# Optimization experiments

Hardware: AMD Instinct MI355X
Metric: run time of the kernel (lower is better)

Reference implementation:

```python
import jax, jax.numpy as jnp
import numpy as np

N_NODES = 100000
N_EDGES = 3200000
N_GRAPHS = 512
DIM_H = 128
N_LAYERS = 3
N_CLASSES = 10
BN_EPS = 1e-5


def setup_inputs() -> dict:
    key = jax.random.key(0)
    ks = jax.random.split(key, 16)
    s = 1.0 / np.sqrt(DIM_H)
    x = jax.random.normal(ks[0], (N_NODES, DIM_H), dtype=jnp.float32)
    edge_index = jax.random.randint(ks[1], (2, N_EDGES), 0, N_NODES, dtype=jnp.int64)
    batch = jnp.sort(jax.random.randint(ks[2], (N_NODES,), 0, N_GRAPHS, dtype=jnp.int64))
    W1 = jax.random.uniform(ks[3], (N_LAYERS, DIM_H, DIM_H), jnp.float32, -s, s)
    b1 = jax.random.uniform(ks[4], (N_LAYERS, DIM_H), jnp.float32, -s, s)
    gamma = jnp.ones((N_LAYERS, DIM_H), jnp.float32)
    beta = jnp.zeros((N_LAYERS, DIM_H), jnp.float32)
    rmean = 0.1 * jax.random.normal(ks[5], (N_LAYERS, DIM_H), dtype=jnp.float32)
    rvar = jax.random.uniform(ks[6], (N_LAYERS, DIM_H), jnp.float32, 0.5, 1.5)
    W2 = jax.random.uniform(ks[7], (N_LAYERS, DIM_H, DIM_H), jnp.float32, -s, s)
    b2 = jax.random.uniform(ks[8], (N_LAYERS, DIM_H), jnp.float32, -s, s)
    dcat = DIM_H * N_LAYERS
    sf = 1.0 / np.sqrt(dcat)
    Wfin = jax.random.uniform(ks[9], (dcat, dcat), jnp.float32, -sf, sf)
    bfin = jax.random.uniform(ks[10], (dcat,), jnp.float32, -sf, sf)
    Wout = jax.random.uniform(ks[11], (dcat, N_CLASSES), jnp.float32, -sf, sf)
    bout = jax.random.uniform(ks[12], (N_CLASSES,), jnp.float32, -sf, sf)
    return {"x": x, "edge_index": edge_index, "batch": batch, "num_layers": N_LAYERS,
            "W1": W1, "b1": b1, "gamma": gamma, "beta": beta, "rmean": rmean, "rvar": rvar,
            "W2": W2, "b2": b2, "Wfin": Wfin, "bfin": bfin, "Wout": Wout, "bout": bout}


def reference(x, edge_index, batch, num_layers, W1, b1, gamma, beta, rmean, rvar, W2, b2, Wfin, bfin, Wout, bout):
    src, dst = edge_index[0], edge_index[1]
    h = x
    pooled = []
    for i in range(num_layers):
        # GINConv (eps=0): MLP(x + sum_{j in N(i)} x_j)
        aggr = jax.ops.segment_sum(h[src], dst, num_segments=N_NODES)
        z = (h + aggr) @ W1[i] + b1[i]
        # BatchNorm1d in eval mode (running stats)
        z = gamma[i] * (z - rmean[i]) * jax.lax.rsqrt(rvar[i] + BN_EPS) + beta[i]
        z = jax.nn.relu(z)
        h = jax.nn.relu(z @ W2[i] + b2[i])
        # global_add_pool: segment-sum over graph ids
        pooled.append(jax.ops.segment_sum(h, batch, num_segments=N_GRAPHS))
    h_fin = jnp.concatenate(pooled, axis=1)  # [G, dim_h*num_layers]
    h_fin = jax.nn.relu(h_fin @ Wfin + bfin)
    # dropout p=0.5 is identity in eval mode
    logits = h_fin @ Wout + bout
    return logits, jax.nn.log_softmax(logits, axis=1)
```

## Files before the change

kernel.cpp:

```cpp
#include <hip/hip_runtime.h>
#include <stdint.h>

#define N_NODES 100000
#define N_EDGES 3200000
#define N_GRAPHS 512
#define DIM 128
#define M_PAD 100096
#define NGB (M_PAD / 256)
#define NBUCK 391
#define CAP 9216
#define TILE 4096
#define NTILE 782
#define XMM_NB 392
#define NPOOL (8 * N_GRAPHS * 384)

typedef __bf16 bf16x8 __attribute__((ext_vector_type(8)));
typedef float f32x4 __attribute__((ext_vector_type(4)));

__device__ __forceinline__ unsigned short f2bf(float f) {
  unsigned u = __float_as_uint(f);
  u = u + 0x7FFFu + ((u >> 16) & 1u);
  return (unsigned short)(u >> 16);
}
__device__ __forceinline__ float bflo(unsigned v) { return __uint_as_float(v << 16); }
__device__ __forceinline__ float bfhi(unsigned v) { return __uint_as_float(v & 0xFFFF0000u); }
__device__ __forceinline__ float bfs(unsigned short v) { return __uint_as_float(((unsigned)v) << 16); }
__device__ __forceinline__ unsigned packbf(float a, float b) {
  return (unsigned)f2bf(a) | ((unsigned)f2bf(b) << 16);
}

__global__ void k_zeroall(int* __restrict__ cnt, int* __restrict__ qbuf,
                          int* __restrict__ pooled) {
  int i = blockIdx.x * 256 + threadIdx.x;
  if (i < NBUCK) cnt[i] = 0;
  if (i < 1024) qbuf[i] = 0;
  if (i < NPOOL) pooled[i] = 0;
}

__global__ __launch_bounds__(256) void k_bucket(const int* __restrict__ ei,
                                                int* __restrict__ cnt,
                                                unsigned* __restrict__ rec) {
  __shared__ int hist[NBUCK];
  __shared__ int curs[NBUCK];
  int t = threadIdx.x;
  int base_e = blockIdx.x * TILE;
  int es[16], ed[16];
#pragma unroll
  for (int k = 0; k < 16; ++k) {
    int e = base_e + k * 256 + t;
    if (e < N_EDGES) { es[k] = ei[e]; ed[k] = ei[N_EDGES + e]; }
    else ed[k] = -1;
  }
  for (int i = t; i < NBUCK; i += 256) hist[i] = 0;
  __syncthreads();
#pragma unroll
  for (int k = 0; k < 16; ++k)
    if (ed[k] >= 0) atomicAdd(&hist[ed[k] >> 8], 1);
  __syncthreads();
  for (int i = t; i < NBUCK; i += 256) {
    int h = hist[i];
    int g = h ? atomicAdd(&cnt[i], h) : 0;
    curs[i] = i * CAP + g;
  }
  __syncthreads();
#pragma unroll
  for (int k = 0; k < 16; ++k) {
    if (ed[k] >= 0) {
      int b = ed[k] >> 8;
      int pos = atomicAdd(&curs[b], 1);
      rec[pos] = ((unsigned)es[k] << 8) | (unsigned)(ed[k] & 255);
    }
  }
}

__global__ __launch_bounds__(512) void k_bscan(const int* __restrict__ cnt,
                                               int* __restrict__ bbase,
                                               int* __restrict__ row_ptr) {
  __shared__ int sc[512];
  int t = threadIdx.x;
  int tot = (t < NBUCK) ? min(cnt[t], CAP) : 0;
  sc[t] = tot; __syncthreads();
  for (int off = 1; off < 512; off <<= 1) {
    int x = (t >= off) ? sc[t - off] : 0;
    __syncthreads();
    sc[t] += x;
    __syncthreads();
  }
  if (t < NBUCK) bbase[t] = sc[t] - tot;
  if (t == NBUCK - 1) {
    bbase[NBUCK] = sc[t];
    row_ptr[N_NODES] = sc[t];
  }
}

__global__ __launch_bounds__(256) void k_build(const unsigned* __restrict__ rec,
                                               const int* __restrict__ cnt,
                                               const int* __restrict__ bbase,
                                               int* __restrict__ row_ptr,
                                               int* __restrict__ col) {
  __shared__ int hist[256];
  __shared__ int sc[256];
  __shared__ int curs[256];
  int b = blockIdx.x, t = threadIdx.x;
  int n = min(cnt[b], CAP);
  const unsigned* p = rec + (size_t)b * CAP;
  hist[t] = 0; __syncthreads();
  for (int i = t; i < n; i += 256) atomicAdd(&hist[p[i] & 255u], 1);
  __syncthreads();
  int v = hist[t];
  sc[t] = v; __syncthreads();
  for (int off = 1; off < 256; off <<= 1) {
    int x = (t >= off) ? sc[t - off] : 0;
    __syncthreads();
    sc[t] += x;
    __syncthreads();
  }
  int excl = bbase[b] + sc[t] - v;
  int node = (b << 8) + t;
  if (node < N_NODES) row_ptr[node] = excl;
  curs[t] = excl;
  __syncthreads();
  for (int i = t; i < n; i += 256) {
    unsigned w = p[i];
    int pos = atomicAdd(&curs[w & 255u], 1);
    col[pos] = (int)(w >> 8);
  }
}

__global__ __launch_bounds__(256) void k_xmm1(const float* __restrict__ x,
                                              float* __restrict__ pmax,
                                              float* __restrict__ pmin) {
  __shared__ float smx[8][32][4];
  __shared__ float smn[8][32][4];
  int t = threadIdx.x;
  int c4 = t & 31;
  int ro = t >> 5;
  float mx0 = 0.f, mx1 = 0.f, mx2 = 0.f, mx3 = 0.f;
  float mn0 = 0.f, mn1 = 0.f, mn2 = 0.f, mn3 = 0.f;
  for (int row = blockIdx.x * 8 + ro; row < N_NODES; row += XMM_NB * 8) {
    float4 v = ((const float4*)x)[(size_t)row * 32 + c4];
    mx0 = fmaxf(mx0, v.x); mn0 = fmaxf(mn0, -v.x);
    mx1 = fmaxf(mx1, v.y); mn1 = fmaxf(mn1, -v.y);
    mx2 = fmaxf(mx2, v.z); mn2 = fmaxf(mn2, -v.z);
    mx3 = fmaxf(mx3, v.w); mn3 = fmaxf(mn3, -v.w);
  }
  smx[ro][c4][0] = mx0; smx[ro][c4][1] = mx1; smx[ro][c4][2] = mx2; smx[ro][c4][3] = mx3;
  smn[ro][c4][0] = mn0; smn[ro][c4][1] = mn1; smn[ro][c4][2] = mn2; smn[ro][c4][3] = mn3;
  __syncthreads();
  for (int off = 4; off > 0; off >>= 1) {
    if (ro < off) {
#pragma unroll
      for (int k = 0; k < 4; ++k) {
        smx[ro][c4][k] = fmaxf(smx[ro][c4][k], smx[ro + off][c4][k]);
        smn[ro][c4][k] = fmaxf(smn[ro][c4][k], smn[ro + off][c4][k]);
      }
    }
    __syncthreads();
  }
  if (ro == 0) {
#pragma unroll
    for (int k = 0; k < 4; ++k) {
      pmax[blockIdx.x * 128 + c4 * 4 + k] = smx[0][c4][k];
      pmin[blockIdx.x * 128 + c4 * 4 + k] = smn[0][c4][k];
    }
  }
}

__global__ __launch_bounds__(64) void k_xmm2(const float* __restrict__ pmax,
                                             const float* __restrict__ pmin,
                                             float* __restrict__ xmx,
                                             float* __restrict__ xminf) {
  int c = blockIdx.x & 127;
  int isMin = blockIdx.x >> 7;
  const float* src = isMin ? pmin : pmax;
  int l = threadIdx.x;
  float m = 0.f;
  for (int p2 = l; p2 < XMM_NB; p2 += 64) m = fmaxf(m, src[p2 * 128 + c]);
#pragma unroll
  for (int off = 32; off > 0; off >>= 1) m = fmaxf(m, __shfl_down(m, off));
  if (l == 0) {
    if (isMin) xminf[c] = -m;
    else xmx[c] = m;
  }
}

__global__ void k_convx(const float* __restrict__ x, const float* __restrict__ qmin,
                        const float* __restrict__ qmax, unsigned short* __restrict__ xq) {
  int j = blockIdx.x * 256 + threadIdx.x;
  if (j >= M_PAD * 32) return;
  int k = j & 31;
  int node = j >> 5;
  unsigned o = 0;
  if (node < N_NODES) {
    float4 f = ((const float4*)x)[j];
    float4 mn = ((const float4*)qmin)[k];
    float4 mx = ((const float4*)qmax)[k];
    float r0 = mx.x - mn.x, r1 = mx.y - mn.y, r2 = mx.z - mn.z, r3 = mx.w - mn.w;
    float is0 = r0 > 1e-20f ? 255.f / r0 : 0.f;
    float is1 = r1 > 1e-20f ? 255.f / r1 : 0.f;
    float is2 = r2 > 1e-20f ? 255.f / r2 : 0.f;
    float is3 = r3 > 1e-20f ? 255.f / r3 : 0.f;
    int q0 = (int)rintf((f.x - mn.x) * is0); q0 = min(max(q0, 0), 255);
    int q1 = (int)rintf((f.y - mn.y) * is1); q1 = min(max(q1, 0), 255);
    int q2 = (int)rintf((f.z - mn.z) * is2); q2 = min(max(q2, 0), 255);
    int q3 = (int)rintf((f.w - mn.w) * is3); q3 = min(max(q3, 0), 255);
    o = (unsigned)q0 | ((unsigned)q1 << 8) | ((unsigned)q2 << 16) | ((unsigned)q3 << 24);
  }
  ((unsigned*)xq)[j] = o;
}

__device__ __forceinline__ unsigned q1dw(unsigned v, float is0, float is1) {
  int q0 = (int)rintf(bflo(v) * is0); q0 = min(max(q0, 0), 255);
  int q1 = (int)rintf(bfhi(v) * is1); q1 = min(max(q1, 0), 255);
  return (unsigned)(q0 | (q1 << 8));
}

__global__ void k_quant(const unsigned* __restrict__ hbf, const float* __restrict__ qmax,
                        unsigned short* __restrict__ hq) {
  int j = blockIdx.x * 256 + threadIdx.x;
  if (j >= M_PAD * 16) return;
  int node = j >> 4;
  uint2 o = make_uint2(0u, 0u);
  if (node < N_NODES) {
    int k = j & 15;
    uint4 v = ((const uint4*)hbf)[j];
    float4 mxa = ((const float4*)qmax)[2 * k];
    float4 mxb = ((const float4*)qmax)[2 * k + 1];
    float ia0 = mxa.x > 1e-20f ? 255.f / mxa.x : 0.f;
    float ia1 = mxa.y > 1e-20f ? 255.f / mxa.y : 0.f;
    float ia2 = mxa.z > 1e-20f ? 255.f / mxa.z : 0.f;
    float ia3 = mxa.w > 1e-20f ? 255.f / mxa.w : 0.f;
    float ib0 = mxb.x > 1e-20f ? 255.f / mxb.x : 0.f;
    float ib1 = mxb.y > 1e-20f ? 255.f / mxb.y : 0.f;
    float ib2 = mxb.z > 1e-20f ? 255.f / mxb.z : 0.f;
    float ib3 = mxb.w > 1e-20f ? 255.f / mxb.w : 0.f;
    o.x = q1dw(v.x, ia0, ia1) | (q1dw(v.y, ia2, ia3) << 16);
    o.y = q1dw(v.z, ib0, ib1) | (q1dw(v.w, ib2, ib3) << 16);
  }
  ((uint2*)hq)[j] = o;
}

__global__ void k_convw(const float* __restrict__ W1, const float* __restrict__ W2,
                        unsigned short* __restrict__ Wt1, unsigned short* __restrict__ Wt2,
                        const float* __restrict__ b1, const float* __restrict__ gamma,
                        const float* __restrict__ beta, const float* __restrict__ rmean,
                        const float* __restrict__ rvar, const float* __restrict__ b2,
                        float* __restrict__ sA1, float* __restrict__ sB1,
                        float* __restrict__ sB2) {
  if (blockIdx.x == 192) {
    for (int i = threadIdx.x; i < 3 * DIM; i += 256) {
      float sa = gamma[i] * rsqrtf(rvar[i] + 1e-5f);
      sA1[i] = sa;
      sB1[i] = fmaf(sa, b1[i] - rmean[i], beta[i]);
      sB2[i] = b2[i];
    }
    return;
  }
  int i = blockIdx.x * 256 + threadIdx.x;
  int l = i >> 14, rem = i & 16383, k = rem >> 7, n = rem & 127;
  int o = (l << 14) + (n << 7) + k;
  Wt1[o] = f2bf(W1[i]);
  Wt2[o] = f2bf(W2[i]);
}

__global__ __launch_bounds__(256) void k_aggr(const unsigned short* __restrict__ hq,
                                              const int* __restrict__ row_ptr,
                                              const int* __restrict__ col,
                                              const float* __restrict__ qmin,
                                              const float* __restrict__ qmax,
                                              unsigned* __restrict__ tmp) {
  const uint4* hq128 = (const uint4*)hq;
  const unsigned* hq32 = (const unsigned*)hq;
  int wv = (blockIdx.x << 2) + (threadIdx.x >> 6);
  int lane = threadIdx.x & 63;
  int grp = lane >> 3;
  int lo8 = lane & 7;
  int dw = lane & 31;
  if (wv >= M_PAD) return;
  if (wv >= N_NODES) {
    ((uint2*)(tmp + (size_t)wv * 64))[dw] = make_uint2(0u, 0u);
    return;
  }
  unsigned ae0 = 0, ae1 = 0, ae2 = 0, ae3 = 0;
  unsigned ao0 = 0, ao1 = 0, ao2 = 0, ao3 = 0;
  int s = __builtin_amdgcn_readfirstlane(row_ptr[wv]);
  int e = __builtin_amdgcn_readfirstlane(row_ptr[wv + 1]);
  int pidx = (lo8 << 3) + grp;
  for (int base = s; base < e; base += 32) {
    int n = e - base; if (n > 32) n = 32;
    int cv = (pidx < n) ? col[base + pidx] : 0;
    int s0 = __builtin_amdgcn_ds_swizzle(cv, 0x18);
    int s1 = __builtin_amdgcn_ds_swizzle(cv, 0x38);
    int s2 = __builtin_amdgcn_ds_swizzle(cv, 0x58);
    int s3 = __builtin_amdgcn_ds_swizzle(cv, 0x78);
    s0 = (grp      < n) ? s0 : N_NODES;
    s1 = (grp +  8 < n) ? s1 : N_NODES;
    s2 = (grp + 16 < n) ? s2 : N_NODES;
    s3 = (grp + 24 < n) ? s3 : N_NODES;
    uint4 v0 = hq128[s0 * 8 + lo8];
    uint4 v1 = hq128[s1 * 8 + lo8];
    uint4 v2 = hq128[s2 * 8 + lo8];
    uint4 v3 = hq128[s3 * 8 + lo8];
    ae0 += v0.x & 0x00FF00FFu; ao0 += (v0.x >> 8) & 0x00FF00FFu;
    ae1 += v0.y & 0x00FF00FFu; ao1 += (v0.y >> 8) & 0x00FF00FFu;
    ae2 += v0.z & 0x00FF00FFu; ao2 += (v0.z >> 8) & 0x00FF00FFu;
    ae3 += v0.w & 0x00FF00FFu; ao3 += (v0.w >> 8) & 0x00FF00FFu;
    ae0 += v1.x & 0x00FF00FFu; ao0 += (v1.x >> 8) & 0x00FF00FFu;
    ae1 += v1.y & 0x00FF00FFu; ao1 += (v1.y >> 8) & 0x00FF00FFu;
    ae2 += v1.z & 0x00FF00FFu; ao2 += (v1.z >> 8) & 0x00FF00FFu;
    ae3 += v1.w & 0x00FF00FFu; ao3 += (v1.w >> 8) & 0x00FF00FFu;
    ae0 += v2.x & 0x00FF00FFu; ao0 += (v2.x >> 8) & 0x00FF00FFu;
    ae1 += v2.y & 0x00FF00FFu; ao1 += (v2.y >> 8) & 0x00FF00FFu;
    ae2 += v2.z & 0x00FF00FFu; ao2 += (v2.z >> 8) & 0x00FF00FFu;
    ae3 += v2.w & 0x00FF00FFu; ao3 += (v2.w >> 8) & 0x00FF00FFu;
    ae0 += v3.x & 0x00FF00FFu; ao0 += (v3.x >> 8) & 0x00FF00FFu;
    ae1 += v3.y & 0x00FF00FFu; ao1 += (v3.y >> 8) & 0x00FF00FFu;
    ae2 += v3.z & 0x00FF00FFu; ao2 += (v3.z >> 8) & 0x00FF00FFu;
    ae3 += v3.w & 0x00FF00FFu; ao3 += (v3.w >> 8) & 0x00FF00FFu;
  }
  ae0 += __shfl_xor(ae0, 8); ae0 += __shfl_xor(ae0, 16); ae0 += __shfl_xor(ae0, 32);
  ae1 += __shfl_xor(ae1, 8); ae1 += __shfl_xor(ae1, 16); ae1 += __shfl_xor(ae1, 32);
  ae2 += __shfl_xor(ae2, 8); ae2 += __shfl_xor(ae2, 16); ae2 += __shfl_xor(ae2, 32);
  ae3 += __shfl_xor(ae3, 8); ae3 += __shfl_xor(ae3, 16); ae3 += __shfl_xor(ae3, 32);
  ao0 += __shfl_xor(ao0, 8); ao0 += __shfl_xor(ao0, 16); ao0 += __shfl_xor(ao0, 32);
  ao1 += __shfl_xor(ao1, 8); ao1 += __shfl_xor(ao1, 16); ao1 += __shfl_xor(ao1, 32);
  ao2 += __shfl_xor(ao2, 8); ao2 += __shfl_xor(ao2, 16); ao2 += __shfl_xor(ao2, 32);
  ao3 += __shfl_xor(ao3, 8); ao3 += __shfl_xor(ao3, 16); ao3 += __shfl_xor(ao3, 32);
  {
    int ba = ((dw >> 2) & 7) << 2;
    unsigned f0 = (unsigned)__builtin_amdgcn_ds_bpermute(ba, (int)ae0);
    unsigned f1 = (unsigned)__builtin_amdgcn_ds_bpermute(ba, (int)ae1);
    unsigned f2 = (unsigned)__builtin_amdgcn_ds_bpermute(ba, (int)ae2);
    unsigned f3 = (unsigned)__builtin_amdgcn_ds_bpermute(ba, (int)ae3);
    unsigned g0 = (unsigned)__builtin_amdgcn_ds_bpermute(ba, (int)ao0);
    unsigned g1 = (unsigned)__builtin_amdgcn_ds_bpermute(ba, (int)ao1);
    unsigned g2 = (unsigned)__builtin_amdgcn_ds_bpermute(ba, (int)ao2);
    unsigned g3 = (unsigned)__builtin_amdgcn_ds_bpermute(ba, (int)ao3);
    unsigned el = (dw & 1) ? f1 : f0;
    unsigned eh = (dw & 1) ? f3 : f2;
    unsigned ae = (dw & 2) ? eh : el;
    unsigned ol = (dw & 1) ? g1 : g0;
    unsigned oh = (dw & 1) ? g3 : g2;
    unsigned ao = (dw & 2) ? oh : ol;
    if (lane < 32) {
      unsigned v = hq32[wv * 32 + dw];
      ae += v & 0x00FF00FFu;
      ao += (v >> 8) & 0x00FF00FFu;
      float cntf = (float)(e - s + 1);
      float4 qn = ((const float4*)qmin)[dw];
      float4 qx = ((const float4*)qmax)[dw];
      const float k255 = 1.0f / 255.0f;
      float A0 = fmaf(qn.x, cntf, (qx.x - qn.x) * k255 * (float)(ae & 0xFFFFu));
      float A1 = fmaf(qn.y, cntf, (qx.y - qn.y) * k255 * (float)(ao & 0xFFFFu));
      float A2 = fmaf(qn.z, cntf, (qx.z - qn.z) * k255 * (float)(ae >> 16));
      float A3 = fmaf(qn.w, cntf, (qx.w - qn.w) * k255 * (float)(ao >> 16));
      ((uint2*)(tmp + (size_t)wv * 64))[dw] = make_uint2(packbf(A0, A1), packbf(A2, A3));
    }
  }
}

__global__ __launch_bounds__(256, 2) void k_gemm12(const unsigned short* __restrict__ A,
                                                   const unsigned short* __restrict__ Wt1,
                                                   const float* __restrict__ sA1,
                                                   const float* __restrict__ sB1,
                                                   const unsigned short* __restrict__ Wt2,
                                                   const float* __restrict__ sB2,
                                                   const int* __restrict__ batch,
                                                   unsigned short* __restrict__ out,
                                                   float* __restrict__ pooled8, int layer,
                                                   float* __restrict__ hmax, int do_max) {
  __shared__ unsigned short zt[4][64][136];
  __shared__ float colred[128];
  __shared__ int sgid[256];
  int w = threadIdx.x >> 6, lane = threadIdx.x & 63;
  int q = lane >> 4, n16 = lane & 15;
  int rbase = (blockIdx.x << 8) + (w << 6);
  if (do_max && threadIdx.x < 128) colred[threadIdx.x] = 0.f;
  {
    int rr = (blockIdx.x << 8) + threadIdx.x;
    sgid[threadIdx.x] = (rr < N_NODES) ? batch[rr] : -1;
  }

  {
    bf16x8 Bf[4][8];
#pragma unroll
    for (int ks = 0; ks < 4; ++ks)
#pragma unroll
      for (int c = 0; c < 8; ++c)
        Bf[ks][c] = *(const bf16x8*)(Wt1 + (size_t)((c << 4) + n16) * DIM + ks * 32 + q * 8);
    bf16x8 an0, an1, an2, an3;
    {
      const unsigned short* ap = A + (size_t)(rbase + n16) * DIM + q * 8;
      an0 = *(const bf16x8*)(ap);
      an1 = *(const bf16x8*)(ap + 32);
      an2 = *(const bf16x8*)(ap + 64);
      an3 = *(const bf16x8*)(ap + 96);
    }
#pragma unroll
    for (int t = 0; t < 4; ++t) {
      bf16x8 a0 = an0, a1 = an1, a2 = an2, a3 = an3;
      if (t < 3) {
        const unsigned short* ap = A + (size_t)(rbase + ((t + 1) << 4) + n16) * DIM + q * 8;
        an0 = *(const bf16x8*)(ap);
        an1 = *(const bf16x8*)(ap + 32);
        an2 = *(const bf16x8*)(ap + 64);
        an3 = *(const bf16x8*)(ap + 96);
      }
      f32x4 acc[8] = {};
#pragma unroll
      for (int c = 0; c < 8; ++c) acc[c] = __builtin_amdgcn_mfma_f32_16x16x32_bf16(a0, Bf[0][c], acc[c], 0, 0, 0);
#pragma unroll
      for (int c = 0; c < 8; ++c) acc[c] = __builtin_amdgcn_mfma_f32_16x16x32_bf16(a1, Bf[1][c], acc[c], 0, 0, 0);
#pragma unroll
      for (int c = 0; c < 8; ++c) acc[c] = __builtin_amdgcn_mfma_f32_16x16x32_bf16(a2, Bf[2][c], acc[c], 0, 0, 0);
#pragma unroll
      for (int c = 0; c < 8; ++c) acc[c] = __builtin_amdgcn_mfma_f32_16x16x32_bf16(a3, Bf[3][c], acc[c], 0, 0, 0);
#pragma unroll
      for (int c = 0; c < 8; ++c) {
        int colc = (c << 4) + n16;
        float s = sA1[colc], tt = sB1[colc];
#pragma unroll
        for (int r = 0; r < 4; ++r) {
          float v = fmaxf(fmaf(s, acc[c][r], tt), 0.0f);
          zt[w][(t << 4) + (q << 2) + r][colc] = f2bf(v);
        }
      }
    }
  }

  float mcol[8];
#pragma unroll
  for (int c = 0; c < 8; ++c) mcol[c] = 0.f;
  {
    bf16x8 Bf[4][8];
#pragma unroll
    for (int ks = 0; ks < 4; ++ks)
#pragma unroll
      for (int c = 0; c < 8; ++c)
        Bf[ks][c] = *(const bf16x8*)(Wt2 + (size_t)((c << 4) + n16) * DIM + ks * 32 + q * 8);
#pragma unroll
    for (int t = 0; t < 4; ++t) {
      f32x4 acc[8] = {};
#pragma unroll
      for (int ks = 0; ks < 4; ++ks) {
        bf16x8 a = *(const bf16x8*)(&zt[w][(t << 4) + n16][ks * 32 + q * 8]);
#pragma unroll
        for (int c = 0; c < 8; ++c)
          acc[c] = __builtin_amdgcn_mfma_f32_16x16x32_bf16(a, Bf[ks][c], acc[c], 0, 0, 0);
      }
      asm volatile("s_waitcnt lgkmcnt(0)" ::: "memory");
#pragma unroll
      for (int c = 0; c < 8; ++c) {
        int colc = (c << 4) + n16;
        float tt = sB2[colc];
#pragma unroll
        for (int r = 0; r < 4; ++r) {
          float v = fmaxf(acc[c][r] + tt, 0.0f);
          mcol[c] = fmaxf(mcol[c], v);
          zt[w][(t << 4) + (q << 2) + r][colc] = f2bf(v);
        }
      }
    }
  }
  __syncthreads();

  if (do_max) {
    const unsigned short* ztf = &zt[0][0][0];
    int chunk = threadIdx.x & 15;
    int rsub  = threadIdx.x >> 4;
    unsigned short* ob = out + ((size_t)blockIdx.x << 8) * DIM;
#pragma unroll
    for (int i = 0; i < 16; ++i) {
      int r = (i << 4) + rsub;
      uint4 v = *(const uint4*)(ztf + r * 136 + chunk * 8);
      *(uint4*)(ob + r * DIM + chunk * 8) = v;
    }
  }

  {
    const unsigned* ztu = (const unsigned*)&zt[0][0][0];
    int cp2 = threadIdx.x & 63;
    int grp = threadIdx.x >> 6;
    int cpy = blockIdx.x & 7;
    float pacc0 = 0.f, pacc1 = 0.f;
    int gcur = sgid[grp << 6];
    for (int r = 0; r < 64; ++r) {
      int row = (grp << 6) + r;
      int g = sgid[row];
      if (g != gcur) {
        if (gcur >= 0) {
          float* bp = &pooled8[((size_t)cpy * N_GRAPHS + gcur) * 384 + layer * DIM + 2 * cp2];
          atomicAdd(bp, pacc0);
          atomicAdd(bp + 1, pacc1);
        }
        pacc0 = 0.f; pacc1 = 0.f; gcur = g;
      }
      if (g >= 0) {
        unsigned v = ztu[row * 68 + cp2];
        pacc0 += bflo(v);
        pacc1 += bfhi(v);
      }
    }
    if (gcur >= 0) {
      float* bp = &pooled8[((size_t)cpy * N_GRAPHS + gcur) * 384 + layer * DIM + 2 * cp2];
      atomicAdd(bp, pacc0);
      atomicAdd(bp + 1, pacc1);
    }
  }

  if (do_max) {
#pragma unroll
    for (int c = 0; c < 8; ++c)
      atomicMax((int*)&colred[(c << 4) + n16], __float_as_int(mcol[c]));
    __syncthreads();
    if (threadIdx.x < 128)
      atomicMax((int*)&hmax[threadIdx.x], __float_as_int(colred[threadIdx.x]));
  }
}

__global__ __launch_bounds__(384) void k_head(const float* __restrict__ pooled8,
                                              const float* __restrict__ Wfin,
                                              const float* __restrict__ bfin,
                                              const float* __restrict__ Wout,
                                              const float* __restrict__ bout,
                                              float* __restrict__ out) {
  __shared__ float p[8][384];
  __shared__ float hf[8][392];
  __shared__ float lg[8][10];
  __shared__ float lse[8];
  int t = threadIdx.x, g0 = blockIdx.x << 3;
  for (int i = t; i < 8 * 384; i += 384) {
    int gl = i / 384, k = i % 384;
    float s = 0.f;
#pragma unroll
    for (int cp = 0; cp < 8; ++cp)
      s += pooled8[((size_t)cp * N_GRAPHS + g0 + gl) * 384 + k];
    p[gl][k] = s;
  }
  __syncthreads();
  float bb = bfin[t];
  float acc[8];
#pragma unroll
  for (int g = 0; g < 8; ++g) acc[g] = bb;
  for (int k = 0; k < 384; ++k) {
    float wv = Wfin[k * 384 + t];
#pragma unroll
    for (int g = 0; g < 8; ++g) acc[g] = fmaf(p[g][k], wv, acc[g]);
  }
#pragma unroll
  for (int g = 0; g < 8; ++g) hf[g][t] = fmaxf(acc[g], 0.f);
  __syncthreads();
  if (t < 80) {
    int g = t / 10, c = t % 10;
    float a = bout[c];
    for (int k = 0; k < 384; ++k) a = fmaf(hf[g][k], Wout[k * 10 + c], a);
    lg[g][c] = a;
  }
  __syncthreads();
  if (t < 8) {
    float m = lg[t][0];
#pragma unroll
    for (int i = 1; i < 10; ++i) m = fmaxf(m, lg[t][i]);
    float ss = 0.f;
#pragma unroll
    for (int i = 0; i < 10; ++i) ss += __expf(lg[t][i] - m);
    lse[t] = m + __logf(ss);
  }
  __syncthreads();
  if (t < 80) {
    int g = t / 10, c = t % 10;
    out[(size_t)(g0 + g) * 10 + c] = lg[g][c];
    out[(size_t)N_GRAPHS * 10 + (size_t)(g0 + g) * 10 + c] = lg[g][c] - lse[g];
  }
}

extern "C" void kernel_launch(void* const* d_in, const int* in_sizes, int n_in,
                              void* d_out, int out_size, void* d_ws, size_t ws_size,
                              hipStream_t stream) {
  const float* x     = (const float*)d_in[0];
  const int*   ei    = (const int*)d_in[1];
  const int*   batch = (const int*)d_in[2];
  const float* W1    = (const float*)d_in[4];
  const float* b1    = (const float*)d_in[5];
  const float* gamma = (const float*)d_in[6];
  const float* beta  = (const float*)d_in[7];
  const float* rmean = (const float*)d_in[8];
  const float* rvar  = (const float*)d_in[9];
  const float* W2    = (const float*)d_in[10];
  const float* b2    = (const float*)d_in[11];
  const float* Wfin  = (const float*)d_in[12];
  const float* bfin  = (const float*)d_in[13];
  const float* Wout  = (const float*)d_in[14];
  const float* bout  = (const float*)d_in[15];
  float* out = (float*)d_out;

  char* p = (char*)d_ws;
  auto alloc = [&](size_t bytes) { char* r = p; p += (bytes + 255) & ~255ull; return r; };
  int* cnt      = (int*)alloc(NBUCK * 4);
  unsigned* rec = (unsigned*)alloc((size_t)NBUCK * CAP * 4);
  int* bbase    = (int*)alloc((NBUCK + 1) * 4);
  int* row_ptr  = (int*)alloc((N_NODES + 1) * 4);
  int* colb     = (int*)alloc(((size_t)N_EDGES + 256) * 4);
  unsigned short* xq  = (unsigned short*)alloc((size_t)M_PAD * 64 * 2);
  unsigned short* hqb = (unsigned short*)alloc((size_t)M_PAD * 64 * 2);
  unsigned* hbf  = (unsigned*)alloc((size_t)M_PAD * 64 * 4);
  unsigned* tmpb = (unsigned*)alloc((size_t)M_PAD * 64 * 4);
  unsigned short* Wt1 = (unsigned short*)alloc(3 * DIM * DIM * 2);
  unsigned short* Wt2 = (unsigned short*)alloc(3 * DIM * DIM * 2);
  float* pmax   = (float*)alloc((size_t)XMM_NB * 128 * 4);
  float* pmin   = (float*)alloc((size_t)XMM_NB * 128 * 4);
  float* sA1    = (float*)alloc(384 * 4);
  float* sB1    = (float*)alloc(384 * 4);
  float* sB2    = (float*)alloc(384 * 4);
  float* qbuf   = (float*)alloc(1024 * 4);
  float* xmx    = qbuf + 128;
  float* xminf  = qbuf + 256;
  float* hmax0  = qbuf + 384;
  float* hmax1  = qbuf + 512;
  float* zeros  = qbuf + 640;
  float* pooled8 = (float*)alloc((size_t)NPOOL * 4);

  k_zeroall<<<(NPOOL + 255) / 256, 256, 0, stream>>>(cnt, (int*)qbuf, (int*)pooled8);

  k_bucket<<<NTILE, 256, 0, stream>>>(ei, cnt, rec);
  k_bscan<<<1, 512, 0, stream>>>(cnt, bbase, row_ptr);
  k_build<<<NBUCK, 256, 0, stream>>>(rec, cnt, bbase, row_ptr, colb);

  k_xmm1<<<XMM_NB, 256, 0, stream>>>(x, pmax, pmin);
  k_xmm2<<<256, 64, 0, stream>>>(pmax, pmin, xmx, xminf);
  k_convx<<<(M_PAD * 32 + 255) / 256, 256, 0, stream>>>(x, xminf, xmx, xq);
  k_convw<<<193, 256, 0, stream>>>(W1, W2, Wt1, Wt2, b1, gamma, beta, rmean, rvar, b2,
                                   sA1, sB1, sB2);

  k_aggr<<<M_PAD / 4, 256, 0, stream>>>(xq, row_ptr, colb, xminf, xmx, tmpb);
  k_gemm12<<<NGB, 256, 0, stream>>>((const unsigned short*)tmpb, Wt1, sA1, sB1,
                                    Wt2, sB2, batch, (unsigned short*)hbf,
                                    pooled8, 0, hmax0, 1);
  k_quant<<<(M_PAD * 16 + 255) / 256, 256, 0, stream>>>(hbf, hmax0, hqb);
  k_aggr<<<M_PAD / 4, 256, 0, stream>>>(hqb, row_ptr, colb, zeros, hmax0, tmpb);
  k_gemm12<<<NGB, 256, 0, stream>>>((const unsigned short*)tmpb, Wt1 + DIM * DIM,
                                    sA1 + DIM, sB1 + DIM, Wt2 + DIM * DIM,
                                    sB2 + DIM, batch, (unsigned short*)hbf,
                                    pooled8, 1, hmax1, 1);
  k_quant<<<(M_PAD * 16 + 255) / 256, 256, 0, stream>>>(hbf, hmax1, hqb);
  k_aggr<<<M_PAD / 4, 256, 0, stream>>>(hqb, row_ptr, colb, zeros, hmax1, tmpb);
  k_gemm12<<<NGB, 256, 0, stream>>>((const unsigned short*)tmpb, Wt1 + 2 * DIM * DIM,
                                    sA1 + 2 * DIM, sB1 + 2 * DIM, Wt2 + 2 * DIM * DIM,
                                    sB2 + 2 * DIM, batch, (unsigned short*)hbf,
                                    pooled8, 2, hmax0, 0);

  k_head<<<N_GRAPHS / 8, 384, 0, stream>>>(pooled8, Wfin, bfin, Wout, bout, out);
}
```

Measured before the change: 556.1 us.

## Merge setup kernels, fold x min/max into atomics, shrink GEMM tile for occupancy

Merges the zeroing and weight conversion kernels into one init kernel. Drops the second min/max reduction pass by having each block atomicMax its partial result, with the sign flip of the min moved into the scan kernel. Restructures the fused GEMM to process 128-row chunks with a half-size shared tile and load weight fragments per half, cutting register and LDS use so three blocks fit per CU. The change removes two kernel launches and raises occupancy, but it reloads the weights from memory for every tile and adds extra barriers.

After: 770.7 us. +38.6%, slower.

```diff
diff --git a/kernel.cpp b/kernel.cpp
--- a/kernel.cpp
+++ b/kernel.cpp
@@ -13,6 +13,7 @@
 #define NTILE 782
 #define XMM_NB 392
 #define NPOOL (8 * N_GRAPHS * 384)
+#define NZB ((NPOOL + 255) / 256)
 
 typedef __bf16 bf16x8 __attribute__((ext_vector_type(8)));
 typedef float f32x4 __attribute__((ext_vector_type(4)));
@@ -29,12 +30,37 @@
   return (unsigned)f2bf(a) | ((unsigned)f2bf(b) << 16);
 }
 
-__global__ void k_zeroall(int* __restrict__ cnt, int* __restrict__ qbuf,
-                          int* __restrict__ pooled) {
-  int i = blockIdx.x * 256 + threadIdx.x;
-  if (i < NBUCK) cnt[i] = 0;
-  if (i < 1024) qbuf[i] = 0;
-  if (i < NPOOL) pooled[i] = 0;
+__global__ void k_init(int* __restrict__ cnt, int* __restrict__ qbuf,
+                       int* __restrict__ pooled,
+                       const float* __restrict__ W1, const float* __restrict__ W2,
+                       unsigned short* __restrict__ Wt1, unsigned short* __restrict__ Wt2,
+                       const float* __restrict__ b1, const float* __restrict__ gamma,
+                       const float* __restrict__ beta, const float* __restrict__ rmean,
+                       const float* __restrict__ rvar, const float* __restrict__ b2,
+                       float* __restrict__ sA1, float* __restrict__ sB1,
+                       float* __restrict__ sB2) {
+  int bid = blockIdx.x;
+  if (bid < NZB) {
+    int i = bid * 256 + threadIdx.x;
+    if (i < NBUCK) cnt[i] = 0;
+    if (i < 1024) qbuf[i] = 0;
+    if (i < NPOOL) pooled[i] = 0;
+    return;
+  }
+  if (bid < NZB + 192) {
+    int i = (bid - NZB) * 256 + threadIdx.x;
+    int l = i >> 14, rem = i & 16383, k = rem >> 7, n = rem & 127;
+    int o = (l << 14) + (n << 7) + k;
+    Wt1[o] = f2bf(W1[i]);
+    Wt2[o] = f2bf(W2[i]);
+    return;
+  }
+  for (int i = threadIdx.x; i < 3 * DIM; i += 256) {
+    float sa = gamma[i] * rsqrtf(rvar[i] + 1e-5f);
+    sA1[i] = sa;
+    sB1[i] = fmaf(sa, b1[i] - rmean[i], beta[i]);
+    sB2[i] = b2[i];
+  }
 }
 
 __global__ __launch_bounds__(256) void k_bucket(const int* __restrict__ ei,
@@ -75,9 +101,11 @@
 
 __global__ __launch_bounds__(512) void k_bscan(const int* __restrict__ cnt,
                                                int* __restrict__ bbase,
-                                               int* __restrict__ row_ptr) {
+                                               int* __restrict__ row_ptr,
+                                               float* __restrict__ xminf) {
   __shared__ int sc[512];
   int t = threadIdx.x;
+  if (t < 128) xminf[t] = -xminf[t];
   int tot = (t < NBUCK) ? min(cnt[t], CAP) : 0;
   sc[t] = tot; __syncthreads();
   for (int off = 1; off < 512; off <<= 1) {
@@ -128,8 +156,8 @@
 }
 
 __global__ __launch_bounds__(256) void k_xmm1(const float* __restrict__ x,
-                                              float* __restrict__ pmax,
-                                              float* __restrict__ pmin) {
+                                              float* __restrict__ xmx,
+                                              float* __restrict__ xminf) {
   __shared__ float smx[8][32][4];
   __shared__ float smn[8][32][4];
   int t = threadIdx.x;
@@ -160,27 +188,9 @@
   if (ro == 0) {
 #pragma unroll
     for (int k = 0; k < 4; ++k) {
-      pmax[blockIdx.x * 128 + c4 * 4 + k] = smx[0][c4][k];
-      pmin[blockIdx.x * 128 + c4 * 4 + k] = smn[0][c4][k];
-    }
-  }
-}
-
-__global__ __launch_bounds__(64) void k_xmm2(const float* __restrict__ pmax,
-                                             const float* __restrict__ pmin,
-                                             float* __restrict__ xmx,
-                                             float* __restrict__ xminf) {
-  int c = blockIdx.x & 127;
-  int isMin = blockIdx.x >> 7;
-  const float* src = isMin ? pmin : pmax;
-  int l = threadIdx.x;
-  float m = 0.f;
-  for (int p2 = l; p2 < XMM_NB; p2 += 64) m = fmaxf(m, src[p2 * 128 + c]);
-#pragma unroll
-  for (int off = 32; off > 0; off >>= 1) m = fmaxf(m, __shfl_down(m, off));
-  if (l == 0) {
-    if (isMin) xminf[c] = -m;
-    else xmx[c] = m;
+      atomicMax((int*)&xmx[c4 * 4 + k], __float_as_int(smx[0][c4][k]));
+      atomicMax((int*)&xminf[c4 * 4 + k], __float_as_int(smn[0][c4][k]));
+    }
   }
 }
 
@@ -238,29 +248,6 @@
     o.y = q1dw(v.z, ib0, ib1) | (q1dw(v.w, ib2, ib3) << 16);
   }
   ((uint2*)hq)[j] = o;
-}
-
-__global__ void k_convw(const float* __restrict__ W1, const float* __restrict__ W2,
-                        unsigned short* __restrict__ Wt1, unsigned short* __restrict__ Wt2,
-                        const float* __restrict__ b1, const float* __restrict__ gamma,
-                        const float* __restrict__ beta, const float* __restrict__ rmean,
-                        const float* __restrict__ rvar, const float* __restrict__ b2,
-                        float* __restrict__ sA1, float* __restrict__ sB1,
-                        float* __restrict__ sB2) {
-  if (blockIdx.x == 192) {
-    for (int i = threadIdx.x; i < 3 * DIM; i += 256) {
-      float sa = gamma[i] * rsqrtf(rvar[i] + 1e-5f);
-      sA1[i] = sa;
-      sB1[i] = fmaf(sa, b1[i] - rmean[i], beta[i]);
-      sB2[i] = b2[i];
-    }
-    return;
-  }
-  int i = blockIdx.x * 256 + threadIdx.x;
-  int l = i >> 14, rem = i & 16383, k = rem >> 7, n = rem & 127;
-  int o = (l << 14) + (n << 7) + k;
-  Wt1[o] = f2bf(W1[i]);
-  Wt2[o] = f2bf(W2[i]);
 }
 
 __global__ __launch_bounds__(256) void k_aggr(const unsigned short* __restrict__ hq,
@@ -359,7 +346,7 @@
   }
 }
 
-__global__ __launch_bounds__(256, 2) void k_gemm12(const unsigned short* __restrict__ A,
+__global__ __launch_bounds__(256, 3) void k_gemm12(const unsigned short* __restrict__ A,
                                                    const unsigned short* __restrict__ Wt1,
                                                    const float* __restrict__ sA1,
                                                    const float* __restrict__ sB1,
@@ -369,52 +356,64 @@
                                                    unsigned short* __restrict__ out,
                                                    float* __restrict__ pooled8, int layer,
                                                    float* __restrict__ hmax, int do_max) {
-  __shared__ unsigned short zt[4][64][136];
+  __shared__ unsigned short zt[4][32][136];
   __shared__ float colred[128];
   __shared__ int sgid[256];
   int w = threadIdx.x >> 6, lane = threadIdx.x & 63;
   int q = lane >> 4, n16 = lane & 15;
-  int rbase = (blockIdx.x << 8) + (w << 6);
   if (do_max && threadIdx.x < 128) colred[threadIdx.x] = 0.f;
   {
     int rr = (blockIdx.x << 8) + threadIdx.x;
     sgid[threadIdx.x] = (rr < N_NODES) ? batch[rr] : -1;
   }
-
-  {
-    bf16x8 Bf[4][8];
-#pragma unroll
-    for (int ks = 0; ks < 4; ++ks)
-#pragma unroll
-      for (int c = 0; c < 8; ++c)
-        Bf[ks][c] = *(const bf16x8*)(Wt1 + (size_t)((c << 4) + n16) * DIM + ks * 32 + q * 8);
-    bf16x8 an0, an1, an2, an3;
-    {
-      const unsigned short* ap = A + (size_t)(rbase + n16) * DIM + q * 8;
-      an0 = *(const bf16x8*)(ap);
-      an1 = *(const bf16x8*)(ap + 32);
-      an2 = *(const bf16x8*)(ap + 64);
-      an3 = *(const bf16x8*)(ap + 96);
-    }
-#pragma unroll
-    for (int t = 0; t < 4; ++t) {
-      bf16x8 a0 = an0, a1 = an1, a2 = an2, a3 = an3;
-      if (t < 3) {
-        const unsigned short* ap = A + (size_t)(rbase + ((t + 1) << 4) + n16) * DIM + q * 8;
-        an0 = *(const bf16x8*)(ap);
-        an1 = *(const bf16x8*)(ap + 32);
-        an2 = *(const bf16x8*)(ap + 64);
-        an3 = *(const bf16x8*)(ap + 96);
+  __syncthreads();
+
+  float mcol[8];
+#pragma unroll
+  for (int c = 0; c < 8; ++c) mcol[c] = 0.f;
+
+  int cp2 = threadIdx.x & 63;
+  int pgrp = threadIdx.x >> 6;
+  int cpy = blockIdx.x & 7;
+  float pacc0 = 0.f, pacc1 = 0.f;
+  int gcur = sgid[pgrp << 5];
+
+#pragma unroll
+  for (int ch = 0; ch < 2; ++ch) {
+    int rbase = (blockIdx.x << 8) + (ch << 7) + (w << 5);
+
+#pragma unroll
+    for (int t = 0; t < 2; ++t) {
+      bf16x8 a0, a1, a2, a3;
+      {
+        const unsigned short* ap = A + (size_t)(rbase + (t << 4) + n16) * DIM + q * 8;
+        a0 = *(const bf16x8*)(ap);
+        a1 = *(const bf16x8*)(ap + 32);
+        a2 = *(const bf16x8*)(ap + 64);
+        a3 = *(const bf16x8*)(ap + 96);
       }
       f32x4 acc[8] = {};
 #pragma unroll
-      for (int c = 0; c < 8; ++c) acc[c] = __builtin_amdgcn_mfma_f32_16x16x32_bf16(a0, Bf[0][c], acc[c], 0, 0, 0);
-#pragma unroll
-      for (int c = 0; c < 8; ++c) acc[c] = __builtin_amdgcn_mfma_f32_16x16x32_bf16(a1, Bf[1][c], acc[c], 0, 0, 0);
-#pragma unroll
-      for (int c = 0; c < 8; ++c) acc[c] = __builtin_amdgcn_mfma_f32_16x16x32_bf16(a2, Bf[2][c], acc[c], 0, 0, 0);
-#pragma unroll
-      for (int c = 0; c < 8; ++c) acc[c] = __builtin_amdgcn_mfma_f32_16x16x32_bf16(a3, Bf[3][c], acc[c], 0, 0, 0);
+      for (int hf = 0; hf < 2; ++hf) {
+        bf16x8 Bf[4][4];
+#pragma unroll
+        for (int ks = 0; ks < 4; ++ks)
+#pragma unroll
+          for (int c = 0; c < 4; ++c)
+            Bf[ks][c] = *(const bf16x8*)(Wt1 + (size_t)(((hf * 4 + c) << 4) + n16) * DIM + ks * 32 + q * 8);
+#pragma unroll
+        for (int c = 0; c < 4; ++c)
+          acc[hf * 4 + c] = __builtin_amdgcn_mfma_f32_16x16x32_bf16(a0, Bf[0][c], acc[hf * 4 + c], 0, 0, 0);
+#pragma unroll
+        for (int c = 0; c < 4; ++c)
+          acc[hf * 4 + c] = __builtin_amdgcn_mfma_f32_16x16x32_bf16(a1, Bf[1][c], acc[hf * 4 + c], 0, 0, 0);
+#pragma unroll
+        for (int c = 0; c < 4; ++c)
+          acc[hf * 4 + c] = __builtin_amdgcn_mfma_f32_16x16x32_bf16(a2, Bf[2][c], acc[hf * 4 + c], 0, 0, 0);
+#pragma unroll
+        for (int c = 0; c < 4; ++c)
+          acc[hf * 4 + c] = __builtin_amdgcn_mfma_f32_16x16x32_bf16(a3, Bf[3][c], acc[hf * 4 + c], 0, 0, 0);
+      }
 #pragma unroll
       for (int c = 0; c < 8; ++c) {
         int colc = (c << 4) + n16;
@@ -426,27 +425,34 @@
         }
       }
     }
-  }
-
-  float mcol[8];
-#pragma unroll
-  for (int c = 0; c < 8; ++c) mcol[c] = 0.f;
-  {
-    bf16x8 Bf[4][8];
-#pragma unroll
-    for (int ks = 0; ks < 4; ++ks)
-#pragma unroll
-      for (int c = 0; c < 8; ++c)
-        Bf[ks][c] = *(const bf16x8*)(Wt2 + (size_t)((c << 4) + n16) * DIM + ks * 32 + q * 8);
-#pragma unroll
-    for (int t = 0; t < 4; ++t) {
+
+#pragma unroll
+    for (int t = 0; t < 2; ++t) {
+      bf16x8 a0 = *(const bf16x8*)(&zt[w][(t << 4) + n16][q * 8]);
+      bf16x8 a1 = *(const bf16x8*)(&zt[w][(t << 4) + n16][32 + q * 8]);
+      bf16x8 a2 = *(const bf16x8*)(&zt[w][(t << 4) + n16][64 + q * 8]);
+      bf16x8 a3 = *(const bf16x8*)(&zt[w][(t << 4) + n16][96 + q * 8]);
       f32x4 acc[8] = {};
 #pragma unroll
-      for (int ks = 0; ks < 4; ++ks) {
-        bf16x8 a = *(const bf16x8*)(&zt[w][(t << 4) + n16][ks * 32 + q * 8]);
-#pragma unroll
-        for (int c = 0; c < 8; ++c)
-          acc[c] = __builtin_amdgcn_mfma_f32_16x16x32_bf16(a, Bf[ks][c], acc[c], 0, 0, 0);
+      for (int hf = 0; hf < 2; ++hf) {
+        bf16x8 Bf[4][4];
+#pragma unroll
+        for (int ks = 0; ks < 4; ++ks)
+#pragma unroll
+          for (int c = 0; c < 4; ++c)
+            Bf[ks][c] = *(const bf16x8*)(Wt2 + (size_t)(((hf * 4 + c) << 4) + n16) * DIM + ks * 32 + q * 8);
+#pragma unroll
+        for (int c = 0; c < 4; ++c)
+          acc[hf * 4 + c] = __builtin_amdgcn_mfma_f32_16x16x32_bf16(a0, Bf[0][c], acc[hf * 4 + c], 0, 0, 0);
+#pragma unroll
+        for (int c = 0; c < 4; ++c)
+          acc[hf * 4 + c] = __builtin_amdgcn_mfma_f32_16x16x32_bf16(a1, Bf[1][c], acc[hf * 4 + c], 0, 0, 0);
+#pragma unroll
+        for (int c = 0; c < 4; ++c)
+          acc[hf * 4 + c] = __builtin_amdgcn_mfma_f32_16x16x32_bf16(a2, Bf[2][c], acc[hf * 4 + c], 0, 0, 0);
+#pragma unroll
+        for (int c = 0; c < 4; ++c)
+          acc[hf * 4 + c] = __builtin_amdgcn_mfma_f32_16x16x32_bf16(a3, Bf[3][c], acc[hf * 4 + c], 0, 0, 0);
       }
       asm volatile("s_waitcnt lgkmcnt(0)" ::: "memory");
 #pragma unroll
@@ -461,51 +467,46 @@
         }
       }
     }
-  }
-  __syncthreads();
-
-  if (do_max) {
-    const unsigned short* ztf = &zt[0][0][0];
-    int chunk = threadIdx.x & 15;
-    int rsub  = threadIdx.x >> 4;
-    unsigned short* ob = out + ((size_t)blockIdx.x << 8) * DIM;
-#pragma unroll
-    for (int i = 0; i < 16; ++i) {
-      int r = (i << 4) + rsub;
-      uint4 v = *(const uint4*)(ztf + r * 136 + chunk * 8);
-      *(uint4*)(ob + r * DIM + chunk * 8) = v;
-    }
-  }
-
-  {
-    const unsigned* ztu = (const unsigned*)&zt[0][0][0];
-    int cp2 = threadIdx.x & 63;
-    int grp = threadIdx.x >> 6;
-    int cpy = blockIdx.x & 7;
-    float pacc0 = 0.f, pacc1 = 0.f;
-    int gcur = sgid[grp << 6];
-    for (int r = 0; r < 64; ++r) {
-      int row = (grp << 6) + r;
-      int g = sgid[row];
-      if (g != gcur) {
-        if (gcur >= 0) {
-          float* bp = &pooled8[((size_t)cpy * N_GRAPHS + gcur) * 384 + layer * DIM + 2 * cp2];
-          atomicAdd(bp, pacc0);
-          atomicAdd(bp + 1, pacc1);
+    __syncthreads();
+
+    if (do_max) {
+      const unsigned short* ztf = &zt[0][0][0];
+      int c16 = threadIdx.x & 15, rsub = threadIdx.x >> 4;
+      unsigned short* ob = out + (size_t)((blockIdx.x << 8) + (ch << 7)) * DIM;
+#pragma unroll
+      for (int i = 0; i < 8; ++i) {
+        int r = (i << 4) + rsub;
+        *(uint4*)(ob + r * DIM + c16 * 8) = *(const uint4*)(ztf + r * 136 + c16 * 8);
+      }
+    }
+
+    {
+      const unsigned* ztu = (const unsigned*)&zt[0][0][0];
+      for (int r = 0; r < 32; ++r) {
+        int rowc = (pgrp << 5) + r;
+        int g = sgid[(ch << 7) + rowc];
+        if (g != gcur) {
+          if (gcur >= 0) {
+            float* bp = &pooled8[((size_t)cpy * N_GRAPHS + gcur) * 384 + layer * DIM + 2 * cp2];
+            atomicAdd(bp, pacc0);
+            atomicAdd(bp + 1, pacc1);
+          }
+          pacc0 = 0.f; pacc1 = 0.f; gcur = g;
         }
-        pacc0 = 0.f; pacc1 = 0.f; gcur = g;
-      }
-      if (g >= 0) {
-        unsigned v = ztu[row * 68 + cp2];
-        pacc0 += bflo(v);
-        pacc1 += bfhi(v);
-      }
-    }
-    if (gcur >= 0) {
-      float* bp = &pooled8[((size_t)cpy * N_GRAPHS + gcur) * 384 + layer * DIM + 2 * cp2];
-      atomicAdd(bp, pacc0);
-      atomicAdd(bp + 1, pacc1);
-    }
+        if (g >= 0) {
+          unsigned v = ztu[rowc * 68 + cp2];
+          pacc0 += bflo(v);
+          pacc1 += bfhi(v);
+        }
+      }
+    }
+    __syncthreads();
+  }
+
+  if (gcur >= 0) {
+    float* bp = &pooled8[((size_t)cpy * N_GRAPHS + gcur) * 384 + layer * DIM + 2 * cp2];
+    atomicAdd(bp, pacc0);
+    atomicAdd(bp + 1, pacc1);
   }
 
   if (do_max) {
@@ -607,8 +608,6 @@
   unsigned* tmpb = (unsigned*)alloc((size_t)M_PAD * 64 * 4);
   unsigned short* Wt1 = (unsigned short*)alloc(3 * DIM * DIM * 2);
   unsigned short* Wt2 = (unsigned short*)alloc(3 * DIM * DIM * 2);
-  float* pmax   = (float*)alloc((size_t)XMM_NB * 128 * 4);
-  float* pmin   = (float*)alloc((size_t)XMM_NB * 128 * 4);
   float* sA1    = (float*)alloc(384 * 4);
   float* sB1    = (float*)alloc(384 * 4);
   float* sB2    = (float*)alloc(384 * 4);
@@ -620,17 +619,18 @@
   float* zeros  = qbuf + 640;
   float* pooled8 = (float*)alloc((size_t)NPOOL * 4);
 
-  k_zeroall<<<(NPOOL + 255) / 256, 256, 0, stream>>>(cnt, (int*)qbuf, (int*)pooled8);
+  k_init<<<NZB + 193, 256, 0, stream>>>(cnt, (int*)qbuf, (int*)pooled8,
+                                        W1, W2, Wt1, Wt2,
+                                        b1, gamma, beta, rmean, rvar, b2,
+                                        sA1, sB1, sB2);
+
+  k_xmm1<<<XMM_NB, 256, 0, stream>>>(x, xmx, xminf);
 
   k_bucket<<<NTILE, 256, 0, stream>>>(ei, cnt, rec);
-  k_bscan<<<1, 512, 0, stream>>>(cnt, bbase, row_ptr);
+  k_bscan<<<1, 512, 0, stream>>>(cnt, bbase, row_ptr, xminf);
   k_build<<<NBUCK, 256, 0, stream>>>(rec, cnt, bbase, row_ptr, colb);
 
-  k_xmm1<<<XMM_NB, 256, 0, stream>>>(x, pmax, pmin);
-  k_xmm2<<<256, 64, 0, stream>>>(pmax, pmin, xmx, xminf);
   k_convx<<<(M_PAD * 32 + 255) / 256, 256, 0, stream>>>(x, xminf, xmx, xq);
-  k_convw<<<193, 256, 0, stream>>>(W1, W2, Wt1, Wt2, b1, gamma, beta, rmean, rvar, b2,
-                                   sA1, sB1, sB2);
 
   k_aggr<<<M_PAD / 4, 256, 0, stream>>>(xq, row_ptr, colb, xminf, xmx, tmpb);
   k_gemm12<<<NGB, 256, 0, stream>>>((const unsigned short*)tmpb, Wt1, sA1, sB1,
```
